# Optimization experiments

Hardware: AMD Instinct MI355X
Metric: run time of the kernel (lower is better)

The kernel has to match this reference:

```python
import jax, jax.numpy as jnp
import numpy as np

B, DIM, L, S, E = 4096, 3, 300, 60, 128
P = L // S  # points per local region = 5


def setup_inputs() -> dict:
    key = jax.random.key(0)
    ks = jax.random.split(key, 9)
    inp = {
        "x": jax.random.normal(ks[0], (B, DIM, L), dtype=jnp.float32),
        # local_emb_nn: Conv1d(DIM, E, 1) -> weight [E, DIM], bias [E]
        "W_le": jax.random.normal(ks[1], (E, DIM), dtype=jnp.float32) * 0.1,
        "b_le": jax.random.normal(ks[2], (E,), dtype=jnp.float32) * 0.1,
        "W_lr": jax.random.normal(ks[3], (S, P), dtype=jnp.float32) * 0.1,
        "b_lr": jax.random.normal(ks[4], (S,), dtype=jnp.float32) * 0.1,
        # global_emb_nn: Conv1d(DIM, E, 1)
        "W_ge": jax.random.normal(ks[5], (E, DIM), dtype=jnp.float32) * 0.1,
        "b_ge": jax.random.normal(ks[6], (E,), dtype=jnp.float32) * 0.1,
        # global_nn: Conv1d(L, 1, 1) -> weight [L], bias scalar
        "W_gn": jax.random.normal(ks[7], (L,), dtype=jnp.float32) * 0.1,
        "b_gn": jax.random.normal(ks[8], (), dtype=jnp.float32) * 0.1,
    }
    return inp


def reference(x, W_le, b_le, W_lr, b_lr, W_ge, b_ge, W_gn, b_gn):
    # global branch: [B,DIM,L] -> [B,E,L] -> relu -> transpose [B,L,E]
    gf = jax.nn.relu(jnp.einsum('ec,bcl->ble', W_ge, x) + b_ge)
    # global_nn: 1x1 conv over L channels -> [B,E], then relu
    gf = jax.nn.relu(jnp.einsum('l,ble->be', W_gn, gf) + b_gn)
    # local branch: [B,DIM,L] -> [B,E,L] -> relu -> transpose [B,L,E]
    lf = jax.nn.relu(jnp.einsum('ec,bcl->ble', W_le, x) + b_le)
    # chunk into S regions of P points, apply per-region 1x1 conv (P->1)
    lf = lf.reshape(B, S, P, E)
    lf = jnp.einsum('sp,bspe->bse', W_lr, lf) + b_lr[None, :, None]
    # add broadcast global feature [B,1,E]
    return lf + gf[:, None, :]
```

## Files before the change

### kernel.cpp

```cpp
#include <hip/hip_runtime.h>


#define Bv 4096
#define Lv 300
#define Sv 60
#define Ev 128

#define RELU(v) fmaxf((v), 0.0f)

__global__ __launch_bounds__(128) void cle_kernel(
    const float* __restrict__ x,
    const float* __restrict__ W_le,
    const float* __restrict__ b_le,
    const float* __restrict__ W_lr,
    const float* __restrict__ b_lr,
    const float* __restrict__ W_ge,
    const float* __restrict__ b_ge,
    const float* __restrict__ W_gn,
    const float* __restrict__ b_gn,
    float* __restrict__ out)
{
    const int e = threadIdx.x;
    const int b = blockIdx.x;

    __shared__ __align__(16) float4 sx4[225];

    {
        const float4* xg4 = (const float4*)(x + (size_t)b * 900);
        for (int i = e; i < 225; i += 128) sx4[i] = xg4[i];
    }

    const float wl0 = W_le[e * 3 + 0], wl1 = W_le[e * 3 + 1], wl2 = W_le[e * 3 + 2];
    const float bl  = b_le[e];
    const float wg0 = W_ge[e * 3 + 0], wg1 = W_ge[e * 3 + 1], wg2 = W_ge[e * 3 + 2];
    const float bg  = b_ge[e];
    const float bgn = b_gn[0];

    __syncthreads();

    float g0 = 0.f, g1 = 0.f, g2 = 0.f, g3 = 0.f;
    float la[60];
#pragma unroll
    for (int i = 0; i < 60; ++i) la[i] = 0.0f;

#define GEq(cmp) RELU(fmaf(wg2, c2.cmp, fmaf(wg1, c1.cmp, fmaf(wg0, c0.cmp, bg))))
#define LEq(cmp) RELU(fmaf(wl2, c2.cmp, fmaf(wl1, c1.cmp, fmaf(wl0, c0.cmp, bl))))
#define DOQ(qi, A0, A1, A2, A3)                                            \
    {                                                                      \
        const int qq = q0 + (qi);                                          \
        const int l4 = qq * 4;                                             \
        const float4 c0 = sx4[qq], c1 = sx4[75 + qq], c2 = sx4[150 + qq];  \
        g0 = fmaf(W_gn[l4 + 0], GEq(x), g0);                               \
        g1 = fmaf(W_gn[l4 + 1], GEq(y), g1);                               \
        g2 = fmaf(W_gn[l4 + 2], GEq(z), g2);                               \
        g3 = fmaf(W_gn[l4 + 3], GEq(w), g3);                               \
        A0 = fmaf(W_lr[l4 + 0], LEq(x), A0);                               \
        A1 = fmaf(W_lr[l4 + 1], LEq(y), A1);                               \
        A2 = fmaf(W_lr[l4 + 2], LEq(z), A2);                               \
        A3 = fmaf(W_lr[l4 + 3], LEq(w), A3);                               \
    }

#pragma unroll
    for (int g = 0; g < 15; ++g) {
        const int q0 = g * 5;
        const int r = 4 * g;
        DOQ(0, la[r + 0], la[r + 0], la[r + 0], la[r + 0])
        DOQ(1, la[r + 0], la[r + 1], la[r + 1], la[r + 1])
        DOQ(2, la[r + 1], la[r + 1], la[r + 2], la[r + 2])
        DOQ(3, la[r + 2], la[r + 2], la[r + 2], la[r + 3])
        DOQ(4, la[r + 3], la[r + 3], la[r + 3], la[r + 3])
    }

    const float gf = RELU(((g0 + g1) + (g2 + g3)) + bgn);

    float* ob = out + (size_t)b * (Sv * Ev) + e;
#pragma unroll
    for (int s = 0; s < 60; ++s) {
        ob[(size_t)s * Ev] = (la[s] + gf) + b_lr[s];
    }
}

extern "C" void kernel_launch(void* const* d_in, const int* in_sizes, int n_in,
                              void* d_out, int out_size, void* d_ws, size_t ws_size,
                              hipStream_t stream) {
    const float* x    = (const float*)d_in[0];
    const float* W_le = (const float*)d_in[1];
    const float* b_le = (const float*)d_in[2];
    const float* W_lr = (const float*)d_in[3];
    const float* b_lr = (const float*)d_in[4];
    const float* W_ge = (const float*)d_in[5];
    const float* b_ge = (const float*)d_in[6];
    const float* W_gn = (const float*)d_in[7];
    const float* b_gn = (const float*)d_in[8];
    float* out = (float*)d_out;

    cle_kernel<<<Bv, Ev, 0, stream>>>(x, W_le, b_le, W_lr, b_lr,
                                      W_ge, b_ge, W_gn, b_gn, out);
}
```

Measured before the change: 50.74 us.

## Split each batch row's L range across four thread groups with shared-memory reduction

Each block now runs 512 threads. Four groups of 128 each handle a quarter of the 15 region groups, so each thread keeps 16 local accumulators instead of 60. The partial global sums are reduced through shared memory after a second barrier. This cuts register pressure and the serial work per thread, which should raise occupancy and parallelism. The cost is an extra sync, one idle quarter-group (the last group only has 3 of 4 region groups), and the global-branch math now being split across groups.

```diff
diff --git a/kernel.cpp b/kernel.cpp
--- a/kernel.cpp
+++ b/kernel.cpp
@@ -2,13 +2,12 @@
 
 
 #define Bv 4096
-#define Lv 300
 #define Sv 60
 #define Ev 128
 
 #define RELU(v) fmaxf((v), 0.0f)
 
-__global__ __launch_bounds__(128) void cle_kernel(
+__global__ __launch_bounds__(512, 8) void cle_kernel(
     const float* __restrict__ x,
     const float* __restrict__ W_le,
     const float* __restrict__ b_le,
@@ -20,14 +19,17 @@
     const float* __restrict__ b_gn,
     float* __restrict__ out)
 {
-    const int e = threadIdx.x;
+    const int tid = threadIdx.x;
+    const int e = tid & 127;
+    const int q = tid >> 7;
     const int b = blockIdx.x;
 
     __shared__ __align__(16) float4 sx4[225];
+    __shared__ float sg[512];
 
     {
         const float4* xg4 = (const float4*)(x + (size_t)b * 900);
-        for (int i = e; i < 225; i += 128) sx4[i] = xg4[i];
+        if (tid < 225) sx4[tid] = xg4[tid];
     }
 
     const float wl0 = W_le[e * 3 + 0], wl1 = W_le[e * 3 + 1], wl2 = W_le[e * 3 + 2];
@@ -38,10 +40,12 @@
 
     __syncthreads();
 
+    const int qb = q * 20;
+
     float g0 = 0.f, g1 = 0.f, g2 = 0.f, g3 = 0.f;
-    float la[60];
+    float la[16];
 #pragma unroll
-    for (int i = 0; i < 60; ++i) la[i] = 0.0f;
+    for (int i = 0; i < 16; ++i) la[i] = 0.0f;
 
 #define GEq(cmp) RELU(fmaf(wg2, c2.cmp, fmaf(wg1, c1.cmp, fmaf(wg0, c0.cmp, bg))))
 #define LEq(cmp) RELU(fmaf(wl2, c2.cmp, fmaf(wl1, c1.cmp, fmaf(wl0, c0.cmp, bl))))
@@ -61,22 +65,34 @@
     }
 
 #pragma unroll
-    for (int g = 0; g < 15; ++g) {
-        const int q0 = g * 5;
-        const int r = 4 * g;
-        DOQ(0, la[r + 0], la[r + 0], la[r + 0], la[r + 0])
-        DOQ(1, la[r + 0], la[r + 1], la[r + 1], la[r + 1])
-        DOQ(2, la[r + 1], la[r + 1], la[r + 2], la[r + 2])
-        DOQ(3, la[r + 2], la[r + 2], la[r + 2], la[r + 3])
-        DOQ(4, la[r + 3], la[r + 3], la[r + 3], la[r + 3])
+    for (int g = 0; g < 4; ++g) {
+        if ((q << 2) + g < 15) {
+            const int q0 = qb + g * 5;
+            const int r = g << 2;
+            DOQ(0, la[r + 0], la[r + 0], la[r + 0], la[r + 0])
+            DOQ(1, la[r + 0], la[r + 1], la[r + 1], la[r + 1])
+            DOQ(2, la[r + 1], la[r + 1], la[r + 2], la[r + 2])
+            DOQ(3, la[r + 2], la[r + 2], la[r + 2], la[r + 3])
+            DOQ(4, la[r + 3], la[r + 3], la[r + 3], la[r + 3])
+        }
     }
 
-    const float gf = RELU(((g0 + g1) + (g2 + g3)) + bgn);
+    sg[tid] = (g0 + g1) + (g2 + g3);
+    __syncthreads();
+    const float gf = RELU((sg[e] + sg[128 + e]) + (sg[256 + e] + sg[384 + e]) + bgn);
 
-    float* ob = out + (size_t)b * (Sv * Ev) + e;
+    float* ob = out + (size_t)b * (Sv * Ev) + (size_t)(q << 4) * Ev + e;
 #pragma unroll
-    for (int s = 0; s < 60; ++s) {
-        ob[(size_t)s * Ev] = (la[s] + gf) + b_lr[s];
+    for (int g = 0; g < 4; ++g) {
+        if ((q << 2) + g < 15) {
+            const int r = g << 2;
+            const int s0 = (q << 4) + (g << 2);
+            float* og = ob + (size_t)(g << 2) * Ev;
+            og[0 * Ev] = la[r + 0] + gf + b_lr[s0 + 0];
+            og[1 * Ev] = la[r + 1] + gf + b_lr[s0 + 1];
+            og[2 * Ev] = la[r + 2] + gf + b_lr[s0 + 2];
+            og[3 * Ev] = la[r + 3] + gf + b_lr[s0 + 3];
+        }
     }
 }
 
@@ -94,6 +110,6 @@
     const float* b_gn = (const float*)d_in[8];
     float* out = (float*)d_out;
 
-    cle_kernel<<<Bv, Ev, 0, stream>>>(x, W_le, b_le, W_lr, b_lr,
-                                      W_ge, b_ge, W_gn, b_gn, out);
+    cle_kernel<<<Bv, 512, 0, stream>>>(x, W_le, b_le, W_lr, b_lr,
+                                       W_ge, b_ge, W_gn, b_gn, out);
 }
```

Result: slower. 93.28 us (+83.8%).

## Use one wave per batch with two channels per thread and float2 stores

Applied to the files above, without the earlier changes.

Each block now has 64 threads, and each thread handles two adjacent embedding channels. The global branch is computed first in its own pass. The local pass then writes each group of four regions right away with float2 stores, instead of holding all 60 accumulators until the end. This cuts register pressure, halves the thread count per batch item, and amortises the shared-memory reads of x over two channels. In exchange, x is read from shared memory twice and per-block parallelism is lower.

```diff
diff --git a/kernel.cpp b/kernel.cpp
--- a/kernel.cpp
+++ b/kernel.cpp
@@ -1,14 +1,9 @@
 #include <hip/hip_runtime.h>
 
 
-#define Bv 4096
-#define Lv 300
-#define Sv 60
-#define Ev 128
-
 #define RELU(v) fmaxf((v), 0.0f)
 
-__global__ __launch_bounds__(128) void cle_kernel(
+__global__ __launch_bounds__(64) void cle_kernel(
     const float* __restrict__ x,
     const float* __restrict__ W_le,
     const float* __restrict__ b_le,
@@ -20,63 +15,89 @@
     const float* __restrict__ b_gn,
     float* __restrict__ out)
 {
-    const int e = threadIdx.x;
+    const int lane = threadIdx.x;
     const int b = blockIdx.x;
+    const int e0 = lane << 1;
 
     __shared__ __align__(16) float4 sx4[225];
 
     {
         const float4* xg4 = (const float4*)(x + (size_t)b * 900);
-        for (int i = e; i < 225; i += 128) sx4[i] = xg4[i];
+        sx4[lane]       = xg4[lane];
+        sx4[lane + 64]  = xg4[lane + 64];
+        sx4[lane + 128] = xg4[lane + 128];
+        if (lane < 33) sx4[lane + 192] = xg4[lane + 192];
     }
 
-    const float wl0 = W_le[e * 3 + 0], wl1 = W_le[e * 3 + 1], wl2 = W_le[e * 3 + 2];
-    const float bl  = b_le[e];
-    const float wg0 = W_ge[e * 3 + 0], wg1 = W_ge[e * 3 + 1], wg2 = W_ge[e * 3 + 2];
-    const float bg  = b_ge[e];
+    const float wg00 = W_ge[e0 * 3 + 0], wg01 = W_ge[e0 * 3 + 1], wg02 = W_ge[e0 * 3 + 2];
+    const float wg10 = W_ge[e0 * 3 + 3], wg11 = W_ge[e0 * 3 + 4], wg12 = W_ge[e0 * 3 + 5];
+    const float bg0 = b_ge[e0], bg1 = b_ge[e0 + 1];
     const float bgn = b_gn[0];
 
     __syncthreads();
 
-    float g0 = 0.f, g1 = 0.f, g2 = 0.f, g3 = 0.f;
-    float la[60];
+    float ga0 = 0.f, ga1 = 0.f, ga2 = 0.f, ga3 = 0.f;
+    float gb0 = 0.f, gb1 = 0.f, gb2 = 0.f, gb3 = 0.f;
+#define GE0(cmp) RELU(fmaf(wg02, c2.cmp, fmaf(wg01, c1.cmp, fmaf(wg00, c0.cmp, bg0))))
+#define GE1(cmp) RELU(fmaf(wg12, c2.cmp, fmaf(wg11, c1.cmp, fmaf(wg10, c0.cmp, bg1))))
+    for (int g = 0; g < 15; ++g) {
+        const int q0 = g * 5;
 #pragma unroll
-    for (int i = 0; i < 60; ++i) la[i] = 0.0f;
+        for (int qi = 0; qi < 5; ++qi) {
+            const int qq = q0 + qi;
+            const int l4 = qq * 4;
+            const float4 c0 = sx4[qq], c1 = sx4[75 + qq], c2 = sx4[150 + qq];
+            ga0 = fmaf(W_gn[l4 + 0], GE0(x), ga0);
+            gb0 = fmaf(W_gn[l4 + 0], GE1(x), gb0);
+            ga1 = fmaf(W_gn[l4 + 1], GE0(y), ga1);
+            gb1 = fmaf(W_gn[l4 + 1], GE1(y), gb1);
+            ga2 = fmaf(W_gn[l4 + 2], GE0(z), ga2);
+            gb2 = fmaf(W_gn[l4 + 2], GE1(z), gb2);
+            ga3 = fmaf(W_gn[l4 + 3], GE0(w), ga3);
+            gb3 = fmaf(W_gn[l4 + 3], GE1(w), gb3);
+        }
+    }
+    const float gf0 = RELU(((ga0 + ga1) + (ga2 + ga3)) + bgn);
+    const float gf1 = RELU(((gb0 + gb1) + (gb2 + gb3)) + bgn);
 
-#define GEq(cmp) RELU(fmaf(wg2, c2.cmp, fmaf(wg1, c1.cmp, fmaf(wg0, c0.cmp, bg))))
-#define LEq(cmp) RELU(fmaf(wl2, c2.cmp, fmaf(wl1, c1.cmp, fmaf(wl0, c0.cmp, bl))))
-#define DOQ(qi, A0, A1, A2, A3)                                            \
-    {                                                                      \
-        const int qq = q0 + (qi);                                          \
-        const int l4 = qq * 4;                                             \
-        const float4 c0 = sx4[qq], c1 = sx4[75 + qq], c2 = sx4[150 + qq];  \
-        g0 = fmaf(W_gn[l4 + 0], GEq(x), g0);                               \
-        g1 = fmaf(W_gn[l4 + 1], GEq(y), g1);                               \
-        g2 = fmaf(W_gn[l4 + 2], GEq(z), g2);                               \
-        g3 = fmaf(W_gn[l4 + 3], GEq(w), g3);                               \
-        A0 = fmaf(W_lr[l4 + 0], LEq(x), A0);                               \
-        A1 = fmaf(W_lr[l4 + 1], LEq(y), A1);                               \
-        A2 = fmaf(W_lr[l4 + 2], LEq(z), A2);                               \
-        A3 = fmaf(W_lr[l4 + 3], LEq(w), A3);                               \
+    const float wl00 = W_le[e0 * 3 + 0], wl01 = W_le[e0 * 3 + 1], wl02 = W_le[e0 * 3 + 2];
+    const float wl10 = W_le[e0 * 3 + 3], wl11 = W_le[e0 * 3 + 4], wl12 = W_le[e0 * 3 + 5];
+    const float bl0 = b_le[e0], bl1 = b_le[e0 + 1];
+
+    float2* ob2 = (float2*)(out + (size_t)b * (60 * 128)) + lane;
+
+#define LE0(cmp) RELU(fmaf(wl02, c2.cmp, fmaf(wl01, c1.cmp, fmaf(wl00, c0.cmp, bl0))))
+#define LE1(cmp) RELU(fmaf(wl12, c2.cmp, fmaf(wl11, c1.cmp, fmaf(wl10, c0.cmp, bl1))))
+#define DOQ(qi, R0, R1, R2, R3)                                                \
+    {                                                                          \
+        const int qq = q0 + (qi);                                              \
+        const int lw = qq * 4;                 \
+        const float4 c0 = sx4[qq], c1 = sx4[75 + qq], c2 = sx4[150 + qq];      \
+        a0##R0 = fmaf(W_lr[lw + 0], LE0(x), a0##R0);                           \
+        a1##R0 = fmaf(W_lr[lw + 0], LE1(x), a1##R0);                           \
+        a0##R1 = fmaf(W_lr[lw + 1], LE0(y), a0##R1);                           \
+        a1##R1 = fmaf(W_lr[lw + 1], LE1(y), a1##R1);                           \
+        a0##R2 = fmaf(W_lr[lw + 2], LE0(z), a0##R2);                           \
+        a1##R2 = fmaf(W_lr[lw + 2], LE1(z), a1##R2);                           \
+        a0##R3 = fmaf(W_lr[lw + 3], LE0(w), a0##R3);                           \
+        a1##R3 = fmaf(W_lr[lw + 3], LE1(w), a1##R3);                           \
     }
 
-#pragma unroll
     for (int g = 0; g < 15; ++g) {
         const int q0 = g * 5;
-        const int r = 4 * g;
-        DOQ(0, la[r + 0], la[r + 0], la[r + 0], la[r + 0])
-        DOQ(1, la[r + 0], la[r + 1], la[r + 1], la[r + 1])
-        DOQ(2, la[r + 1], la[r + 1], la[r + 2], la[r + 2])
-        DOQ(3, la[r + 2], la[r + 2], la[r + 2], la[r + 3])
-        DOQ(4, la[r + 3], la[r + 3], la[r + 3], la[r + 3])
-    }
+        float a00 = 0.f, a01 = 0.f, a02 = 0.f, a03 = 0.f;
+        float a10 = 0.f, a11 = 0.f, a12 = 0.f, a13 = 0.f;
+        DOQ(0, 0, 0, 0, 0)
+        DOQ(1, 0, 1, 1, 1)
+        DOQ(2, 1, 1, 2, 2)
+        DOQ(3, 2, 2, 2, 3)
+        DOQ(4, 3, 3, 3, 3)
 
-    const float gf = RELU(((g0 + g1) + (g2 + g3)) + bgn);
-
-    float* ob = out + (size_t)b * (Sv * Ev) + e;
-#pragma unroll
-    for (int s = 0; s < 60; ++s) {
-        ob[(size_t)s * Ev] = (la[s] + gf) + b_lr[s];
+        const int s0 = g * 4;
+        ob2[(s0 + 0) * 64] = make_float2(a00 + gf0 + b_lr[s0 + 0], a10 + gf1 + b_lr[s0 + 0]);
+        ob2[(s0 + 1) * 64] = make_float2(a01 + gf0 + b_lr[s0 + 1], a11 + gf1 + b_lr[s0 + 1]);
+        ob2[(s0 + 2) * 64] = make_float2(a02 + gf0 + b_lr[s0 + 2], a12 + gf1 + b_lr[s0 + 2]);
+        ob2[(s0 + 3) * 64] = make_float2(a03 + gf0 + b_lr[s0 + 3], a13 + gf1 + b_lr[s0 + 3]);
     }
 }
 
@@ -94,6 +115,6 @@
     const float* b_gn = (const float*)d_in[8];
     float* out = (float*)d_out;
 
-    cle_kernel<<<Bv, Ev, 0, stream>>>(x, W_le, b_le, W_lr, b_lr,
-                                      W_ge, b_ge, W_gn, b_gn, out);
+    cle_kernel<<<4096, 64, 0, stream>>>(x, W_le, b_le, W_lr, b_lr,
+                                        W_ge, b_ge, W_gn, b_gn, out);
 }
```

New measurement: 46.52 us. 1.09x faster.
